# Kernel optimization log

Measured on AMD Instinct MI355X. Metric: run time of the kernel, lower is better.

The kernel has to match this reference:

```python
import jax, jax.numpy as jnp
import numpy as np

EPS_DEN = 1e-6
EPS_LN = 1e-6


def setup_inputs() -> dict:
    key = jax.random.key(0)
    ks = jax.random.split(key, 10)
    B, H, NH = 64, 2048, 8
    HD = H // NH
    q = jax.random.normal(ks[0], (B, 1, H), jnp.float32)
    k = jax.random.normal(ks[1], (B, 1, H), jnp.float32)
    v = jax.random.normal(ks[2], (B, 1, H), jnp.float32)
    c = jax.random.normal(ks[3], (B, NH, HD, HD), jnp.float32)
    n = jax.random.normal(ks[4], (B, NH, HD, 1), jnp.float32)
    m = jnp.zeros((B, NH, 1, 1), jnp.float32)
    wi_kernel = 0.01 * jax.random.normal(ks[5], (3 * H, NH), jnp.float32)
    wi_bias = 0.1 * jax.random.normal(ks[6], (NH,), jnp.float32)
    wf_kernel = 0.01 * jax.random.normal(ks[7], (3 * H, NH), jnp.float32)
    wf_bias = jnp.linspace(3.0, 6.0, NH, dtype=jnp.float32)  # linspace_init(3,6)
    ln_scale = jnp.ones((NH, HD), jnp.float32)
    return {"q": q, "k": k, "v": v, "c": c, "n": n, "m": m,
            "wi_kernel": wi_kernel, "wi_bias": wi_bias,
            "wf_kernel": wf_kernel, "wf_bias": wf_bias, "ln_scale": ln_scale}


def reference(q, k, v, c, n, m, wi_kernel, wi_bias, wf_kernel, wf_bias, ln_scale):
    B, S, H = q.shape            # S == 1 (single-step cell)
    NH, HD = ln_scale.shape
    qkv = jnp.concatenate([q, k, v], axis=-1)           # (B,1,3H)
    qh = q.reshape(B, NH, HD, S)                        # (B,NH,HD,1)
    kh = k.reshape(B, NH, HD, S) / jnp.sqrt(jnp.asarray(HD, q.dtype))
    vh = v.reshape(B, NH, HD, S)
    # gates: Dense(3H -> NH), then (B,1,NH) -> (B,NH,1,1)
    i_tilde = (qkv @ wi_kernel + wi_bias).swapaxes(-1, -2)[..., None]
    f_tilde = (qkv @ wf_kernel + wf_bias).swapaxes(-1, -2)[..., None]
    log_f = -jax.nn.softplus(-f_tilde)                  # log sigmoid(f_tilde)
    m_new = jnp.maximum(log_f + m, i_tilde)             # log-domain stabilizer
    i_prime = jnp.exp(i_tilde - m_new)
    f_prime = jnp.exp(log_f + m - m_new)
    c_new = f_prime * c + i_prime * (kh @ vh.swapaxes(-1, -2))   # (B,NH,HD,HD)
    n_new = f_prime * n + i_prime * kh                            # (B,NH,HD,1)
    nominator = qh.swapaxes(-1, -2) @ c_new                       # (B,NH,1,HD)
    denominator = jnp.maximum(jnp.abs(qh.swapaxes(-1, -2) @ n_new), jnp.exp(-m_new))
    h_tilde = nominator / (denominator + EPS_DEN)                 # (B,NH,1,HD)
    # MultiHeadLayerNorm: normalize over head_dim, per-head scale, no bias
    mu = h_tilde.mean(-1, keepdims=True)
    var = h_tilde.var(-1, keepdims=True)
    h_norm = (h_tilde - mu) * jax.lax.rsqrt(var + EPS_LN) * ln_scale[None, :, None, :]
    h_norm = h_norm.swapaxes(1, 2).reshape(B, S, -1)              # (B,1,H)
    return (c_new, n_new, m_new, h_norm)
```

## Files before the change

### kernel.cpp

```cpp
#include <hip/hip_runtime.h>
#include <math.h>

typedef float f32x4 __attribute__((ext_vector_type(4)));

constexpr int Bb  = 64;
constexpr int Hh  = 2048;
constexpr int NHh = 8;
constexpr int HDd = 256;

constexpr size_t C_OFF = 0;
constexpr size_t N_OFF = (size_t)Bb * NHh * HDd * HDd;
constexpr size_t M_OFF = N_OFF + (size_t)Bb * NHh * HDd;
constexpr size_t H_OFF = M_OFF + (size_t)Bb * NHh;

__global__ __launch_bounds__(256) void gates_kernel(
    const float* __restrict__ q, const float* __restrict__ k,
    const float* __restrict__ v, const float* __restrict__ n_in,
    const float* __restrict__ m_in,
    const float* __restrict__ wi_k, const float* __restrict__ wi_b,
    const float* __restrict__ wf_k, const float* __restrict__ wf_b,
    float* __restrict__ ws, float* __restrict__ out)
{
    const int b    = blockIdx.x;
    const int t    = threadIdx.x;
    const int lane = t & 63;
    const int wv   = t >> 6;

    {
        f32x4 z = {0.f, 0.f, 0.f, 0.f};
        f32x4* zp = (f32x4*)(out + H_OFF + (size_t)b * Hh) + t * 2;
        zp[0] = z; zp[1] = z;
    }

    float ai[8], af[8];
#pragma unroll
    for (int i = 0; i < 8; ++i) { ai[i] = 0.f; af[i] = 0.f; }

#pragma unroll 4
    for (int j = 0; j < 24; ++j) {
        const int r = t + 256 * j;
        float x;
        if (r < Hh)            x = q[b * Hh + r];
        else if (r < 2 * Hh)   x = k[b * Hh + r - Hh];
        else                   x = v[b * Hh + r - 2 * Hh];

        const f32x4 wa = *(const f32x4*)(wi_k + (size_t)r * 8);
        const f32x4 wb = *(const f32x4*)(wi_k + (size_t)r * 8 + 4);
        ai[0] = fmaf(x, wa[0], ai[0]); ai[1] = fmaf(x, wa[1], ai[1]);
        ai[2] = fmaf(x, wa[2], ai[2]); ai[3] = fmaf(x, wa[3], ai[3]);
        ai[4] = fmaf(x, wb[0], ai[4]); ai[5] = fmaf(x, wb[1], ai[5]);
        ai[6] = fmaf(x, wb[2], ai[6]); ai[7] = fmaf(x, wb[3], ai[7]);

        const f32x4 fa = *(const f32x4*)(wf_k + (size_t)r * 8);
        const f32x4 fb = *(const f32x4*)(wf_k + (size_t)r * 8 + 4);
        af[0] = fmaf(x, fa[0], af[0]); af[1] = fmaf(x, fa[1], af[1]);
        af[2] = fmaf(x, fa[2], af[2]); af[3] = fmaf(x, fa[3], af[3]);
        af[4] = fmaf(x, fb[0], af[4]); af[5] = fmaf(x, fb[1], af[5]);
        af[6] = fmaf(x, fb[2], af[6]); af[7] = fmaf(x, fb[3], af[7]);
    }

#pragma unroll
    for (int i = 0; i < 8; ++i) {
#pragma unroll
        for (int o = 32; o > 0; o >>= 1) {
            ai[i] += __shfl_down(ai[i], o, 64);
            af[i] += __shfl_down(af[i], o, 64);
        }
    }

    __shared__ float s_part[4][16];
    __shared__ float s_g[8][3];
    if (lane == 0) {
#pragma unroll
        for (int i = 0; i < 8; ++i) {
            s_part[wv][i]     = ai[i];
            s_part[wv][8 + i] = af[i];
        }
    }
    __syncthreads();

    if (t < 8) {
        const int h = t;
        const float it = s_part[0][h] + s_part[1][h] + s_part[2][h] + s_part[3][h]
                         + wi_b[h];
        const float ft = s_part[0][8 + h] + s_part[1][8 + h] + s_part[2][8 + h]
                         + s_part[3][8 + h] + wf_b[h];
        const float logf_ = -(fmaxf(-ft, 0.f) + log1pf(expf(-fabsf(ft))));
        const float m_old = m_in[b * NHh + h];
        const float m_new = fmaxf(logf_ + m_old, it);
        const float fp    = expf(logf_ + m_old - m_new);
        const float ip    = expf(it - m_new);
        const int blk = b * NHh + h;
        s_g[h][0] = fp; s_g[h][1] = ip; s_g[h][2] = m_new;
        ws[blk * 4 + 0] = fp;
        ws[blk * 4 + 1] = ip;
        ws[blk * 4 + 2] = m_new;
        out[M_OFF + blk] = m_new;
    }
    __syncthreads();

    float pd[8];
#pragma unroll
    for (int h = 0; h < 8; ++h) {
        const float kv = k[b * Hh + h * HDd + t] * 0.0625f;
        const float nn = fmaf(s_g[h][0], n_in[((size_t)b * 8 + h) * HDd + t],
                              s_g[h][1] * kv);
        out[N_OFF + ((size_t)b * 8 + h) * HDd + t] = nn;
        pd[h] = q[b * Hh + h * HDd + t] * nn;
    }
#pragma unroll
    for (int h = 0; h < 8; ++h)
#pragma unroll
        for (int o = 32; o > 0; o >>= 1) pd[h] += __shfl_down(pd[h], o, 64);

    __shared__ float s_dp[4][8];
    if (lane == 0) {
#pragma unroll
        for (int h = 0; h < 8; ++h) s_dp[wv][h] = pd[h];
    }
    __syncthreads();
    if (t < 8) {
        const float dd = s_dp[0][t] + s_dp[1][t] + s_dp[2][t] + s_dp[3][t];
        ws[(b * 8 + t) * 4 + 3] = fmaxf(fabsf(dd), expf(-s_g[t][2])) + 1e-6f;
    }
}

__global__ __launch_bounds__(256) void stream_kernel(
    const float* __restrict__ q, const float* __restrict__ k,
    const float* __restrict__ v, const float* __restrict__ c_in,
    const float* __restrict__ ws, float* __restrict__ out)
{
    const int blk  = blockIdx.x;
    const int tile = blk >> 3;
    const int s    = blk & 7;
    const int b    = tile >> 3;
    const int h    = tile & 7;
    const int t    = threadIdx.x;
    const int lane = t & 63;
    const int wv   = t >> 6;

    __shared__ float s_kh[32];
    __shared__ float s_qh[32];
    __shared__ f32x4 s_nom[4][64];

    if (t < 32) {
        const int r = s * 32 + t;
        s_kh[t] = k[b * Hh + h * HDd + r] * 0.0625f;
        s_qh[t] = q[b * Hh + h * HDd + r];
    }
    const float fp  = ws[tile * 4 + 0];
    const float ip  = ws[tile * 4 + 1];
    const f32x4 vh4 = ((const f32x4*)(v + b * Hh + h * HDd))[lane];
    __syncthreads();

    const size_t cbase = (size_t)tile * (HDd * HDd);
    const f32x4* cin   = (const f32x4*)(c_in + cbase);
    f32x4*       cout  = (f32x4*)(out + C_OFF + cbase);
    f32x4 nom = {0.f, 0.f, 0.f, 0.f};
    const int rb = wv * 8;

#pragma unroll
    for (int j = 0; j < 8; ++j) {
        const int   r   = rb + j;
        const float a   = ip * s_kh[r];
        const float qh1 = s_qh[r];
        const int   idx = (s * 32 + r) * 64 + lane;
        f32x4 cv = __builtin_nontemporal_load(cin + idx);
        f32x4 cn = fp * cv + a * vh4;
        __builtin_nontemporal_store(cn, cout + idx);
        nom += qh1 * cn;
    }
    s_nom[wv][lane] = nom;
    __syncthreads();

    if (t < 64) {
        f32x4 sum = s_nom[0][t] + s_nom[1][t] + s_nom[2][t] + s_nom[3][t];
        float* dst = out + H_OFF + (size_t)tile * HDd + t * 4;
        atomicAdd(dst + 0, sum[0]);
        atomicAdd(dst + 1, sum[1]);
        atomicAdd(dst + 2, sum[2]);
        atomicAdd(dst + 3, sum[3]);
    }
}

__global__ __launch_bounds__(64) void ln_kernel(
    const float* __restrict__ ln_s, const float* __restrict__ ws,
    float* __restrict__ out)
{
    const int blk  = blockIdx.x;
    const int h    = blk & 7;
    const int lane = threadIdx.x;

    float* hp = out + H_OFF + (size_t)blk * HDd;
    const f32x4 nt   = ((const f32x4*)hp)[lane];
    const float rden = 1.f / ws[blk * 4 + 3];
    f32x4 ht = nt * rden;

    float s = ht[0] + ht[1] + ht[2] + ht[3];
#pragma unroll
    for (int o = 32; o > 0; o >>= 1) s += __shfl_down(s, o, 64);
    s = __shfl(s, 0, 64);
    const float mu = s * (1.f / 256.f);

    const f32x4 d = ht - mu;
    float vs = d[0] * d[0] + d[1] * d[1] + d[2] * d[2] + d[3] * d[3];
#pragma unroll
    for (int o = 32; o > 0; o >>= 1) vs += __shfl_down(vs, o, 64);
    vs = __shfl(vs, 0, 64);
    const float rs = rsqrtf(vs * (1.f / 256.f) + 1e-6f);

    const f32x4 lns = ((const f32x4*)(ln_s + h * HDd))[lane];
    ((f32x4*)hp)[lane] = d * rs * lns;
}

extern "C" void kernel_launch(void* const* d_in, const int* in_sizes, int n_in,
                              void* d_out, int out_size, void* d_ws, size_t ws_size,
                              hipStream_t stream)
{
    const float* q    = (const float*)d_in[0];
    const float* k    = (const float*)d_in[1];
    const float* v    = (const float*)d_in[2];
    const float* c    = (const float*)d_in[3];
    const float* n    = (const float*)d_in[4];
    const float* m    = (const float*)d_in[5];
    const float* wi_k = (const float*)d_in[6];
    const float* wi_b = (const float*)d_in[7];
    const float* wf_k = (const float*)d_in[8];
    const float* wf_b = (const float*)d_in[9];
    const float* ln_s = (const float*)d_in[10];
    float* out = (float*)d_out;
    float* ws  = (float*)d_ws;

    gates_kernel<<<dim3(Bb), dim3(256), 0, stream>>>(
        q, k, v, n, m, wi_k, wi_b, wf_k, wf_b, ws, out);
    stream_kernel<<<dim3(Bb * NHh * 8), dim3(256), 0, stream>>>(
        q, k, v, c, ws, out);
    ln_kernel<<<dim3(Bb * NHh), dim3(64), 0, stream>>>(ln_s, ws, out);
}
```

Measured before the change: 262.3 us.

## Replace atomic h accumulation with per-slice partials and batch C loads

The stream kernel now covers 64 rows per block instead of 32, halving the block count, and issues all 16 C loads per thread before any compute, using regular loads in place of nontemporal ones. Float atomics into the output are replaced by per-slice partial sums written to workspace, which the layer-norm kernel adds up. This also removes the zero-initialisation of the h output in the gates kernel. The cost is higher register pressure from 16 vector loads in flight, plus extra workspace traffic for the partials.

After: 274.6 us. 4.7% more time.

```diff
diff --git a/kernel.cpp b/kernel.cpp
--- a/kernel.cpp
+++ b/kernel.cpp
@@ -12,6 +12,8 @@
 constexpr size_t N_OFF = (size_t)Bb * NHh * HDd * HDd;
 constexpr size_t M_OFF = N_OFF + (size_t)Bb * NHh * HDd;
 constexpr size_t H_OFF = M_OFF + (size_t)Bb * NHh;
+
+constexpr size_t PS = 4096;
 
 __global__ __launch_bounds__(256) void gates_kernel(
     const float* __restrict__ q, const float* __restrict__ k,
@@ -25,12 +27,6 @@
     const int t    = threadIdx.x;
     const int lane = t & 63;
     const int wv   = t >> 6;
-
-    {
-        f32x4 z = {0.f, 0.f, 0.f, 0.f};
-        f32x4* zp = (f32x4*)(out + H_OFF + (size_t)b * Hh) + t * 2;
-        zp[0] = z; zp[1] = z;
-    }
 
     float ai[8], af[8];
 #pragma unroll
@@ -125,61 +121,60 @@
     }
 }
 
-__global__ __launch_bounds__(256) void stream_kernel(
+__global__ __launch_bounds__(256, 4) void stream_kernel(
     const float* __restrict__ q, const float* __restrict__ k,
     const float* __restrict__ v, const float* __restrict__ c_in,
-    const float* __restrict__ ws, float* __restrict__ out)
+    const float* __restrict__ ws_r, float* __restrict__ ws_w,
+    float* __restrict__ out)
 {
     const int blk  = blockIdx.x;
-    const int tile = blk >> 3;
-    const int s    = blk & 7;
+    const int tile = blk >> 2;
+    const int s    = blk & 3;
     const int b    = tile >> 3;
     const int h    = tile & 7;
     const int t    = threadIdx.x;
     const int lane = t & 63;
     const int wv   = t >> 6;
 
-    __shared__ float s_kh[32];
-    __shared__ float s_qh[32];
+    __shared__ float s_kh[64];
+    __shared__ float s_qh[64];
     __shared__ f32x4 s_nom[4][64];
 
-    if (t < 32) {
-        const int r = s * 32 + t;
+    if (t < 64) {
+        const int r = s * 64 + t;
         s_kh[t] = k[b * Hh + h * HDd + r] * 0.0625f;
         s_qh[t] = q[b * Hh + h * HDd + r];
     }
-    const float fp  = ws[tile * 4 + 0];
-    const float ip  = ws[tile * 4 + 1];
+    const float fp  = ws_r[tile * 4 + 0];
+    const float ip  = ws_r[tile * 4 + 1];
     const f32x4 vh4 = ((const f32x4*)(v + b * Hh + h * HDd))[lane];
     __syncthreads();
 
     const size_t cbase = (size_t)tile * (HDd * HDd);
     const f32x4* cin   = (const f32x4*)(c_in + cbase);
     f32x4*       cout  = (f32x4*)(out + C_OFF + cbase);
+    const int    l0    = wv * 16;
+    const int    g0    = s * 64 + l0;
+
+    f32x4 cv[16];
+#pragma unroll
+    for (int j = 0; j < 16; ++j)
+        cv[j] = cin[(g0 + j) * 64 + lane];
+
     f32x4 nom = {0.f, 0.f, 0.f, 0.f};
-    const int rb = wv * 8;
-
-#pragma unroll
-    for (int j = 0; j < 8; ++j) {
-        const int   r   = rb + j;
-        const float a   = ip * s_kh[r];
-        const float qh1 = s_qh[r];
-        const int   idx = (s * 32 + r) * 64 + lane;
-        f32x4 cv = __builtin_nontemporal_load(cin + idx);
-        f32x4 cn = fp * cv + a * vh4;
-        __builtin_nontemporal_store(cn, cout + idx);
-        nom += qh1 * cn;
+#pragma unroll
+    for (int j = 0; j < 16; ++j) {
+        const int   lr = l0 + j;
+        const f32x4 cn = fp * cv[j] + (ip * s_kh[lr]) * vh4;
+        __builtin_nontemporal_store(cn, cout + (size_t)(g0 + j) * 64 + lane);
+        nom += s_qh[lr] * cn;
     }
     s_nom[wv][lane] = nom;
     __syncthreads();
 
     if (t < 64) {
-        f32x4 sum = s_nom[0][t] + s_nom[1][t] + s_nom[2][t] + s_nom[3][t];
-        float* dst = out + H_OFF + (size_t)tile * HDd + t * 4;
-        atomicAdd(dst + 0, sum[0]);
-        atomicAdd(dst + 1, sum[1]);
-        atomicAdd(dst + 2, sum[2]);
-        atomicAdd(dst + 3, sum[3]);
+        const f32x4 sum = s_nom[0][t] + s_nom[1][t] + s_nom[2][t] + s_nom[3][t];
+        ((f32x4*)(ws_w + PS))[(size_t)blk * 64 + t] = sum;
     }
 }
 
@@ -191,10 +186,14 @@
     const int h    = blk & 7;
     const int lane = threadIdx.x;
 
-    float* hp = out + H_OFF + (size_t)blk * HDd;
-    const f32x4 nt   = ((const f32x4*)hp)[lane];
+    const f32x4* pp = (const f32x4*)(ws + PS);
+    f32x4 nt = {0.f, 0.f, 0.f, 0.f};
+#pragma unroll
+    for (int s = 0; s < 4; ++s)
+        nt += pp[((size_t)blk * 4 + s) * 64 + lane];
+
     const float rden = 1.f / ws[blk * 4 + 3];
-    f32x4 ht = nt * rden;
+    const f32x4 ht   = nt * rden;
 
     float s = ht[0] + ht[1] + ht[2] + ht[3];
 #pragma unroll
@@ -210,7 +209,7 @@
     const float rs = rsqrtf(vs * (1.f / 256.f) + 1e-6f);
 
     const f32x4 lns = ((const f32x4*)(ln_s + h * HDd))[lane];
-    ((f32x4*)hp)[lane] = d * rs * lns;
+    ((f32x4*)(out + H_OFF + (size_t)blk * HDd))[lane] = d * rs * lns;
 }
 
 extern "C" void kernel_launch(void* const* d_in, const int* in_sizes, int n_in,
@@ -233,7 +232,7 @@
 
     gates_kernel<<<dim3(Bb), dim3(256), 0, stream>>>(
         q, k, v, n, m, wi_k, wi_b, wf_k, wf_b, ws, out);
-    stream_kernel<<<dim3(Bb * NHh * 8), dim3(256), 0, stream>>>(
-        q, k, v, c, ws, out);
+    stream_kernel<<<dim3(Bb * NHh * 4), dim3(256), 0, stream>>>(
+        q, k, v, c, ws, ws, out);
     ln_kernel<<<dim3(Bb * NHh), dim3(64), 0, stream>>>(ln_s, ws, out);
 }
```
